# Kernel tuning notes

Measured on AMD Instinct MI355X. Metric: run time of the kernel, lower is better.

The kernel has to match this reference:

```python
import jax, jax.numpy as jnp
import numpy as np

N_HEAD = 12

def setup_inputs() -> dict:
    key = jax.random.key(0)
    ks = jax.random.split(key, 6)
    B, T, C, P = 8, 1024, 768, 4
    s = 0.02
    return {
        "x": jax.random.normal(ks[0], (B, T, C), jnp.float32),
        "kv_cvec": jax.random.normal(ks[1], (B, P, 2 * C), jnp.float32),
        "w_attn": jax.random.normal(ks[2], (C, 3 * C), jnp.float32) * s,
        "b_attn": jax.random.normal(ks[3], (3 * C,), jnp.float32) * s,
        "w_proj": jax.random.normal(ks[4], (C, C), jnp.float32) * s,
        "b_proj": jax.random.normal(ks[5], (C,), jnp.float32) * s,
    }

def reference(x, kv_cvec, w_attn, b_attn, w_proj, b_proj):
    B, T, C = x.shape
    P = kv_cvec.shape[1]
    D = C // N_HEAD

    # fused QKV projection
    qkv = x @ w_attn + b_attn                       # [B, T, 3C]
    q, k, v = jnp.split(qkv, 3, axis=-1)

    def to_heads(t):  # [B, S, C] -> [B, H, S, D]
        return t.reshape(t.shape[0], t.shape[1], N_HEAD, D).transpose(0, 2, 1, 3)

    q, k, v = to_heads(q), to_heads(k), to_heads(v)

    # prepend prefix (cvec) keys/values -> kv length T+P
    k_cvec, v_cvec = jnp.split(kv_cvec, 2, axis=-1)  # [B, P, C] each
    k = jnp.concatenate([to_heads(k_cvec), k], axis=2)
    v = jnp.concatenate([to_heads(v_cvec), v], axis=2)

    scale = 1.0 / jnp.sqrt(jnp.asarray(D, dtype=x.dtype))
    scores = jnp.einsum('bhqd,bhkd->bhqk', q, k) * scale  # [B,H,T,T+P]

    # mask: prefix columns fully visible, rest causal
    qi = jnp.arange(T)[:, None]
    kj = jnp.arange(T + P)[None, :]
    mask = (kj < P) | ((kj - P) <= qi)                     # [T, T+P]
    scores = jnp.where(mask, scores, jnp.finfo(scores.dtype).min)

    attn = jax.nn.softmax(scores, axis=-1)
    y = jnp.einsum('bhqk,bhkd->bhqd', attn, v)             # [B,H,T,D]
    y = y.transpose(0, 2, 1, 3).reshape(B, T, C)
    return y @ w_proj + b_proj
```

## Files before the change

### kernel.cpp

```cpp
#include <hip/hip_runtime.h>

#define BB 8
#define TT 1024
#define CC 768
#define HH 12
#define DD 64
#define PP 4
#define SS 1028
#define SP 1056

typedef unsigned short u16;
typedef __bf16 bf16x8 __attribute__((ext_vector_type(8)));
typedef unsigned short u16x8 __attribute__((ext_vector_type(8)));
typedef unsigned short u16x4 __attribute__((ext_vector_type(4)));
typedef float f32x4 __attribute__((ext_vector_type(4)));

__device__ __forceinline__ u16 f2bf(float f) {
  unsigned u = __float_as_uint(f);
  u += 0x7FFFu + ((u >> 16) & 1u);
  return (u16)(u >> 16);
}

__device__ __forceinline__ bf16x8 ldfrag(const u16* p) {
  u16x8 v = *reinterpret_cast<const u16x8*>(p);
  return __builtin_bit_cast(bf16x8, v);
}

__device__ __forceinline__ void gload16(const void* g, void* l) {
  __builtin_amdgcn_global_load_lds(
      (const __attribute__((address_space(1))) char*)g,
      (__attribute__((address_space(3))) char*)l, 16, 0, 0);
}

__global__ __launch_bounds__(256) void k_cast_x(const float* __restrict__ x,
                                                u16* __restrict__ xb) {
  int i = (blockIdx.x * 256 + threadIdx.x) * 8;
  float4 a = *reinterpret_cast<const float4*>(x + i);
  float4 b = *reinterpret_cast<const float4*>(x + i + 4);
  u16x8 o;
  o[0] = f2bf(a.x); o[1] = f2bf(a.y); o[2] = f2bf(a.z); o[3] = f2bf(a.w);
  o[4] = f2bf(b.x); o[5] = f2bf(b.y); o[6] = f2bf(b.z); o[7] = f2bf(b.w);
  *reinterpret_cast<u16x8*>(xb + i) = o;
}

__global__ __launch_bounds__(256) void k_transw(const float* __restrict__ w,
                                                u16* __restrict__ wt,
                                                int R, int Cc) {
  __shared__ u16 t[32][33];
  int tx = threadIdx.x & 31, ty = threadIdx.x >> 5;
  int r0 = blockIdx.y * 32, c0 = blockIdx.x * 32;
#pragma unroll
  for (int j = 0; j < 4; ++j) {
    int r = r0 + ty * 4 + j;
    t[ty * 4 + j][tx] = f2bf(w[(size_t)r * Cc + c0 + tx]);
  }
  __syncthreads();
#pragma unroll
  for (int j = 0; j < 4; ++j) {
    int c = c0 + ty * 4 + j;
    wt[(size_t)c * R + r0 + tx] = t[tx][ty * 4 + j];
  }
}

__global__ __launch_bounds__(256) void k_prefix(const float* __restrict__ kv,
                                                u16* __restrict__ Ko,
                                                u16* __restrict__ Vo) {
  int idx = blockIdx.x * 256 + threadIdx.x;
  int which = idx >= (BB * PP * CC);
  int r = idx - which * (BB * PP * CC);
  int b = r / (PP * CC);
  int rem = r - b * (PP * CC);
  int p = rem / CC, c = rem - (rem / CC) * CC;
  int h = c >> 6, d = c & 63;
  float v = kv[(size_t)(b * PP + p) * (2 * CC) + which * CC + c];
  u16* dst = which ? Vo : Ko;
  dst[((size_t)(b * HH + h) * SP + p) * DD + d] = f2bf(v);
}

__global__ __launch_bounds__(256) void k_transv(const u16* __restrict__ V,
                                                u16* __restrict__ VT) {
  __shared__ u16 t[32][33];
  int tx = threadIdx.x & 31, ty = threadIdx.x >> 5;
  int bh = blockIdx.x >> 1, dt = blockIdx.x & 1;
  int s0 = blockIdx.y * 32;
  const u16* src = V + (size_t)bh * SP * DD;
  u16* dst = VT + (size_t)bh * DD * SP;
#pragma unroll
  for (int j = 0; j < 4; ++j)
    t[ty * 4 + j][tx] = src[(size_t)(s0 + ty * 4 + j) * DD + dt * 32 + tx];
  __syncthreads();
#pragma unroll
  for (int j = 0; j < 4; ++j)
    dst[(size_t)(dt * 32 + ty * 4 + j) * SP + s0 + tx] = t[tx][ty * 4 + j];
}

template <int MODE>
__global__ __launch_bounds__(256) void k_gemm(const u16* __restrict__ A,
                                              const u16* __restrict__ Bt,
                                              const float* __restrict__ bias,
                                              u16* __restrict__ Qo,
                                              u16* __restrict__ Ko,
                                              u16* __restrict__ Vo,
                                              float* __restrict__ Fo) {
  __shared__ u16 S[16384];
  u16* const As = S;
  u16* const Bs = S + 8192;

  const int tid = threadIdx.x;
  const int lane = tid & 63, wave = tid >> 6;
  const int wr = wave >> 1, wc = wave & 1;
  const int fr = lane & 15, fq = lane >> 4;
  const int mbase = blockIdx.x * 128, nbase = blockIdx.y * 128;
  const int n0 = nbase + wc * 64;

  f32x4 acc[4][4] = {};

  const int srow = wave * 32 + (lane >> 3);
  const int scol = (lane & 7) * 8;
  const u16* Ag = A + (size_t)(mbase + srow) * 768 + scol;
  const u16* Bg = Bt + (size_t)(nbase + srow) * 768 + scol;
  u16* const Asw = As + (wave * 32) * 64;
  u16* const Bsw = Bs + (wave * 32) * 64;

  for (int kt = 0; kt < 12; ++kt) {
#pragma unroll
    for (int j = 0; j < 4; ++j) {
      gload16(Ag + (size_t)j * 8 * 768 + kt * 64, Asw + j * 8 * 64);
      gload16(Bg + (size_t)j * 8 * 768 + kt * 64, Bsw + j * 8 * 64);
    }
    __syncthreads();
#pragma unroll
    for (int ks = 0; ks < 2; ++ks) {
      bf16x8 av[4], bv[4];
#pragma unroll
      for (int mi = 0; mi < 4; ++mi)
        av[mi] = ldfrag(As + (wr * 64 + mi * 16 + fr) * 64 + ks * 32 + fq * 8);
#pragma unroll
      for (int ni = 0; ni < 4; ++ni)
        bv[ni] = ldfrag(Bs + (wc * 64 + ni * 16 + fr) * 64 + ks * 32 + fq * 8);
#pragma unroll
      for (int mi = 0; mi < 4; ++mi)
#pragma unroll
        for (int ni = 0; ni < 4; ++ni)
          acc[mi][ni] = __builtin_amdgcn_mfma_f32_16x16x32_bf16(
              av[mi], bv[ni], acc[mi][ni], 0, 0, 0);
    }
    __syncthreads();
  }

  float bvl[4];
#pragma unroll
  for (int ni = 0; ni < 4; ++ni) bvl[ni] = bias[n0 + ni * 16 + fr];

  if (MODE == 0) {
    char* const W = (char*)S + wave * 4608;
    const int sec = n0 / 768;
    const int hd = (n0 - sec * 768) >> 6;
    u16* const base = (sec == 0) ? Qo : (sec == 1 ? Ko : Vo);
    const int sstr = (sec == 0) ? TT : SP;
    const int soff = (sec == 0) ? 0 : PP;
#pragma unroll
    for (int p = 0; p < 2; ++p) {
#pragma unroll
      for (int mi2 = 0; mi2 < 2; ++mi2)
#pragma unroll
        for (int ni = 0; ni < 4; ++ni)
#pragma unroll
          for (int i = 0; i < 4; ++i) {
            int lr = mi2 * 16 + fq * 4 + i;
            *(u16*)(W + lr * 144 + (ni * 16 + fr) * 2) =
                f2bf(acc[p * 2 + mi2][ni][i] + bvl[ni]);
          }
#pragma unroll
      for (int it = 0; it < 4; ++it) {
        int lr = it * 8 + (lane >> 3);
        u16x8 v = *(u16x8*)(W + lr * 144 + (lane & 7) * 16);
        int m = mbase + wr * 64 + p * 32 + lr;
        int b = m >> 10, t = m & 1023;
        *(u16x8*)(base + ((size_t)(b * HH + hd) * sstr + soff + t) * DD +
                  (lane & 7) * 8) = v;
      }
    }
  } else {
    char* const W = (char*)S + wave * 4352;
#pragma unroll
    for (int p = 0; p < 4; ++p) {
#pragma unroll
      for (int ni = 0; ni < 4; ++ni)
#pragma unroll
        for (int i = 0; i < 4; ++i) {
          int lr = fq * 4 + i;
          *(float*)(W + lr * 272 + (ni * 16 + fr) * 4) = acc[p][ni][i] + bvl[ni];
        }
#pragma unroll
      for (int it = 0; it < 4; ++it) {
        int lr = it * 4 + (lane >> 4);
        f32x4 v = *(f32x4*)(W + lr * 272 + (lane & 15) * 16);
        int m = mbase + wr * 64 + p * 16 + lr;
        *(f32x4*)(Fo + (size_t)m * 768 + n0 + (lane & 15) * 4) = v;
      }
    }
  }
}

__global__ __launch_bounds__(256) void k_attn(const u16* __restrict__ Q,
                                              const u16* __restrict__ K,
                                              const u16* __restrict__ VT,
                                              u16* __restrict__ Y) {
  __shared__ u16 Ks[2][4096];
  __shared__ u16 Vs[2][4096];
  __shared__ u16 Ps[4][2048];

  const int tid = threadIdx.x;
  const int lane = tid & 63, wave = tid >> 6;
  const int fr = lane & 15, fq = lane >> 4;
  const int tier = blockIdx.x / 96;
  const int bh = blockIdx.x - tier * 96;
  const int tile = 7 - tier;
  const int b = bh / HH, h = bh - b * HH;
  const int qw = tile * 128 + wave * 32;
  const int nblk = 2 * tile + 3;

  const u16* Qb = Q + ((size_t)bh * TT + qw) * DD;
  const u16* Kb = K + (size_t)bh * SP * DD;
  const u16* Vb = VT + (size_t)bh * DD * SP;

  bf16x8 qB[2][2];
#pragma unroll
  for (int qf = 0; qf < 2; ++qf)
#pragma unroll
    for (int ks = 0; ks < 2; ++ks)
      qB[qf][ks] = ldfrag(Qb + (size_t)(qf * 16 + fr) * DD + ks * 32 + fq * 8);

  f32x4 oacc[2][4] = {};
  float mrun[2] = {-1e30f, -1e30f};
  float lrun[2] = {0.f, 0.f};
  const float CSC = 0.125f * 1.44269504f;

  auto stage = [&](int buf, int kv0) {
#pragma unroll
    for (int i = 0; i < 2; ++i) {
      int g = i * 4 + wave;
      int t = g >> 1, ks = g & 1;
      int row = kv0 + t * 16 + fr;
      if (row > SP - 1) row = SP - 1;
      gload16(Kb + (size_t)row * DD + ks * 32 + fq * 8, &Ks[buf][g * 512]);
    }
#pragma unroll
    for (int i = 0; i < 2; ++i) {
      int g = i * 4 + wave;
      int dc = g >> 1, kc = g & 1;
      int col = kv0 + kc * 32 + fq * 8;
      if (col > SP - 8) col = SP - 8;
      gload16(Vb + (size_t)(dc * 16 + fr) * SP + col, &Vs[buf][g * 512]);
    }
  };

  stage(0, 0);
  __syncthreads();

  for (int blk = 0; blk < nblk; ++blk) {
    const int cur = blk & 1;
    const int kv0 = blk * 64;
    if (blk + 1 < nblk) stage(cur ^ 1, kv0 + 64);

    const bool active = (kv0 <= qw + 31 + PP);
    if (active) {
      f32x4 s[2][4] = {};
#pragma unroll
      for (int t = 0; t < 4; ++t) {
        bf16x8 k0 = ldfrag(&Ks[cur][(t * 2 + 0) * 512 + lane * 8]);
        bf16x8 k1 = ldfrag(&Ks[cur][(t * 2 + 1) * 512 + lane * 8]);
#pragma unroll
        for (int qf = 0; qf < 2; ++qf) {
          s[qf][t] = __builtin_amdgcn_mfma_f32_16x16x32_bf16(k0, qB[qf][0], s[qf][t], 0, 0, 0);
          s[qf][t] = __builtin_amdgcn_mfma_f32_16x16x32_bf16(k1, qB[qf][1], s[qf][t], 0, 0, 0);
        }
      }

      const bool needmask = (kv0 + 63 > qw + PP);
#pragma unroll
      for (int qf = 0; qf < 2; ++qf) {
        const int qrow = qw + qf * 16 + fr;
        if (needmask) {
#pragma unroll
          for (int t = 0; t < 4; ++t)
#pragma unroll
            for (int i = 0; i < 4; ++i) {
              int col = kv0 + t * 16 + fq * 4 + i;
              if (col > qrow + PP) s[qf][t][i] = -1e30f;
            }
        }
        float m16 = s[qf][0][0];
#pragma unroll
        for (int t = 0; t < 4; ++t)
#pragma unroll
          for (int i = 0; i < 4; ++i) m16 = fmaxf(m16, s[qf][t][i]);
        m16 = fmaxf(m16, __shfl_xor(m16, 16));
        m16 = fmaxf(m16, __shfl_xor(m16, 32));
        const float mnew = fmaxf(mrun[qf], m16);
        const float alr = __builtin_exp2f((mrun[qf] - mnew) * CSC);
        mrun[qf] = mnew;
        const float mc = mnew * CSC;

        float rs = 0.f;
#pragma unroll
        for (int t = 0; t < 4; ++t) {
          u16x4 w4;
#pragma unroll
          for (int i = 0; i < 4; ++i) {
            float p = __builtin_exp2f(fmaf(s[qf][t][i], CSC, -mc));
            rs += p;
            w4[i] = f2bf(p);
          }
          int off = (qf * 2 + (t >> 1)) * 512 + ((t & 1) * 2 + (fq >> 1)) * 128 +
                    fr * 8 + (fq & 1) * 4;
          *reinterpret_cast<u16x4*>(&Ps[wave][off]) = w4;
        }
        rs += __shfl_xor(rs, 16);
        rs += __shfl_xor(rs, 32);
        lrun[qf] = lrun[qf] * alr + rs;

        float a0 = __shfl(alr, fq * 4 + 0);
        float a1 = __shfl(alr, fq * 4 + 1);
        float a2 = __shfl(alr, fq * 4 + 2);
        float a3 = __shfl(alr, fq * 4 + 3);
#pragma unroll
        for (int dc = 0; dc < 4; ++dc) {
          oacc[qf][dc][0] *= a0;
          oacc[qf][dc][1] *= a1;
          oacc[qf][dc][2] *= a2;
          oacc[qf][dc][3] *= a3;
        }
      }

      asm volatile("s_waitcnt lgkmcnt(0)" ::: "memory");
      bf16x8 pa[2][2];
#pragma unroll
      for (int qf = 0; qf < 2; ++qf)
#pragma unroll
        for (int kc = 0; kc < 2; ++kc)
          pa[qf][kc] = ldfrag(&Ps[wave][(qf * 2 + kc) * 512 + lane * 8]);
#pragma unroll
      for (int kc = 0; kc < 2; ++kc)
#pragma unroll
        for (int dc = 0; dc < 4; ++dc) {
          bf16x8 vf = ldfrag(&Vs[cur][(dc * 2 + kc) * 512 + lane * 8]);
#pragma unroll
          for (int qf = 0; qf < 2; ++qf)
            oacc[qf][dc] = __builtin_amdgcn_mfma_f32_16x16x32_bf16(
                pa[qf][kc], vf, oacc[qf][dc], 0, 0, 0);
        }
    }
    __syncthreads();
  }

#pragma unroll
  for (int qf = 0; qf < 2; ++qf) {
    float l0 = 1.f / __shfl(lrun[qf], fq * 4 + 0);
    float l1 = 1.f / __shfl(lrun[qf], fq * 4 + 1);
    float l2 = 1.f / __shfl(lrun[qf], fq * 4 + 2);
    float l3 = 1.f / __shfl(lrun[qf], fq * 4 + 3);
#pragma unroll
    for (int dc = 0; dc < 4; ++dc) {
      int q0 = qw + qf * 16 + fq * 4;
      u16* yp = Y + ((size_t)b * TT + q0) * CC + h * DD + dc * 16 + fr;
      yp[0 * CC] = f2bf(oacc[qf][dc][0] * l0);
      yp[1 * CC] = f2bf(oacc[qf][dc][1] * l1);
      yp[2 * CC] = f2bf(oacc[qf][dc][2] * l2);
      yp[3 * CC] = f2bf(oacc[qf][dc][3] * l3);
    }
  }
}

extern "C" void kernel_launch(void* const* d_in, const int* in_sizes, int n_in,
                              void* d_out, int out_size, void* d_ws, size_t ws_size,
                              hipStream_t stream) {
  const float* x      = (const float*)d_in[0];
  const float* kv     = (const float*)d_in[1];
  const float* w_attn = (const float*)d_in[2];
  const float* b_attn = (const float*)d_in[3];
  const float* w_proj = (const float*)d_in[4];
  const float* b_proj = (const float*)d_in[5];
  float* out = (float*)d_out;

  char* ws = (char*)d_ws;
  u16* xb  = (u16*)(ws + 0);
  u16* wat = (u16*)(ws + 12582912);
  u16* wpt = (u16*)(ws + 16121856);
  u16* Qb  = (u16*)(ws + 17301504);
  u16* Kb  = (u16*)(ws + 29884416);
  u16* Vb  = (u16*)(ws + 42860544);
  u16* VTb = (u16*)(ws + 55836672);
  u16* Yb  = (u16*)(ws + 68812800);

  k_cast_x<<<3072, 256, 0, stream>>>(x, xb);
  k_transw<<<dim3(72, 24), 256, 0, stream>>>(w_attn, wat, 768, 2304);
  k_transw<<<dim3(24, 24), 256, 0, stream>>>(w_proj, wpt, 768, 768);
  k_gemm<0><<<dim3(64, 18), 256, 0, stream>>>(xb, wat, b_attn, Qb, Kb, Vb, nullptr);
  k_prefix<<<192, 256, 0, stream>>>(kv, Kb, Vb);
  k_transv<<<dim3(192, 33), 256, 0, stream>>>(Vb, VTb);
  k_attn<<<768, 256, 0, stream>>>(Qb, Kb, VTb, Yb);
  k_gemm<1><<<dim3(64, 6), 256, 0, stream>>>(Yb, wpt, b_proj, nullptr, nullptr, nullptr, out);
}
```

Baseline: 216.8 us.

## Load K/V fragments directly from global memory and defer softmax rescaling in attention

The attention kernel no longer stages K and V tiles through double-buffered shared memory with block-wide barriers. Each wave now loads its MFMA fragments straight from global memory (relying on L2/L1 caching) and uses its own per-wave block count, so waves with shorter causal ranges stop early. It also skips the running-max rescale unless the new block max exceeds the old one by a threshold, and uses the hardware bf16 conversion. The risk is global-load latency that is no longer hidden by explicit prefetch, plus redundant global traffic across the four waves.

```diff
diff --git a/kernel.cpp b/kernel.cpp
--- a/kernel.cpp
+++ b/kernel.cpp
@@ -19,6 +19,11 @@
   unsigned u = __float_as_uint(f);
   u += 0x7FFFu + ((u >> 16) & 1u);
   return (u16)(u >> 16);
+}
+
+__device__ __forceinline__ u16 f2bf_fast(float f) {
+  __bf16 h = (__bf16)f;
+  return __builtin_bit_cast(u16, h);
 }
 
 __device__ __forceinline__ bf16x8 ldfrag(const u16* p) {
@@ -207,8 +212,6 @@
                                               const u16* __restrict__ K,
                                               const u16* __restrict__ VT,
                                               u16* __restrict__ Y) {
-  __shared__ u16 Ks[2][4096];
-  __shared__ u16 Vs[2][4096];
   __shared__ u16 Ps[4][2048];
 
   const int tid = threadIdx.x;
@@ -219,7 +222,7 @@
   const int tile = 7 - tier;
   const int b = bh / HH, h = bh - b * HH;
   const int qw = tile * 128 + wave * 32;
-  const int nblk = 2 * tile + 3;
+  const int nblk = (qw + 98) >> 6;
 
   const u16* Qb = Q + ((size_t)bh * TT + qw) * DD;
   const u16* Kb = K + (size_t)bh * SP * DD;
@@ -236,91 +239,51 @@
   float mrun[2] = {-1e30f, -1e30f};
   float lrun[2] = {0.f, 0.f};
   const float CSC = 0.125f * 1.44269504f;
-
-  auto stage = [&](int buf, int kv0) {
-#pragma unroll
-    for (int i = 0; i < 2; ++i) {
-      int g = i * 4 + wave;
-      int t = g >> 1, ks = g & 1;
-      int row = kv0 + t * 16 + fr;
-      if (row > SP - 1) row = SP - 1;
-      gload16(Kb + (size_t)row * DD + ks * 32 + fq * 8, &Ks[buf][g * 512]);
-    }
-#pragma unroll
-    for (int i = 0; i < 2; ++i) {
-      int g = i * 4 + wave;
-      int dc = g >> 1, kc = g & 1;
-      int col = kv0 + kc * 32 + fq * 8;
-      if (col > SP - 8) col = SP - 8;
-      gload16(Vb + (size_t)(dc * 16 + fr) * SP + col, &Vs[buf][g * 512]);
-    }
-  };
-
-  stage(0, 0);
-  __syncthreads();
+  const float THRN = 8.0f / CSC;
+  u16* const plw = Ps[wave];
 
   for (int blk = 0; blk < nblk; ++blk) {
-    const int cur = blk & 1;
     const int kv0 = blk * 64;
-    if (blk + 1 < nblk) stage(cur ^ 1, kv0 + 64);
-
-    const bool active = (kv0 <= qw + 31 + PP);
-    if (active) {
-      f32x4 s[2][4] = {};
-#pragma unroll
-      for (int t = 0; t < 4; ++t) {
-        bf16x8 k0 = ldfrag(&Ks[cur][(t * 2 + 0) * 512 + lane * 8]);
-        bf16x8 k1 = ldfrag(&Ks[cur][(t * 2 + 1) * 512 + lane * 8]);
-#pragma unroll
-        for (int qf = 0; qf < 2; ++qf) {
-          s[qf][t] = __builtin_amdgcn_mfma_f32_16x16x32_bf16(k0, qB[qf][0], s[qf][t], 0, 0, 0);
-          s[qf][t] = __builtin_amdgcn_mfma_f32_16x16x32_bf16(k1, qB[qf][1], s[qf][t], 0, 0, 0);
-        }
-      }
-
-      const bool needmask = (kv0 + 63 > qw + PP);
+
+    f32x4 s[2][4] = {};
+#pragma unroll
+    for (int t = 0; t < 4; ++t) {
+      const u16* kr = Kb + (size_t)(kv0 + t * 16 + fr) * DD + fq * 8;
+      bf16x8 k0 = ldfrag(kr);
+      bf16x8 k1 = ldfrag(kr + 32);
 #pragma unroll
       for (int qf = 0; qf < 2; ++qf) {
-        const int qrow = qw + qf * 16 + fr;
-        if (needmask) {
-#pragma unroll
-          for (int t = 0; t < 4; ++t)
-#pragma unroll
-            for (int i = 0; i < 4; ++i) {
-              int col = kv0 + t * 16 + fq * 4 + i;
-              if (col > qrow + PP) s[qf][t][i] = -1e30f;
-            }
-        }
-        float m16 = s[qf][0][0];
+        s[qf][t] = __builtin_amdgcn_mfma_f32_16x16x32_bf16(k0, qB[qf][0], s[qf][t], 0, 0, 0);
+        s[qf][t] = __builtin_amdgcn_mfma_f32_16x16x32_bf16(k1, qB[qf][1], s[qf][t], 0, 0, 0);
+      }
+    }
+
+    const bool needmask = (kv0 + 63 > qw + PP);
+#pragma unroll
+    for (int qf = 0; qf < 2; ++qf) {
+      const int qrow = qw + qf * 16 + fr;
+      if (needmask) {
 #pragma unroll
         for (int t = 0; t < 4; ++t)
 #pragma unroll
-          for (int i = 0; i < 4; ++i) m16 = fmaxf(m16, s[qf][t][i]);
-        m16 = fmaxf(m16, __shfl_xor(m16, 16));
-        m16 = fmaxf(m16, __shfl_xor(m16, 32));
+          for (int i = 0; i < 4; ++i) {
+            int col = kv0 + t * 16 + fq * 4 + i;
+            if (col > qrow + PP) s[qf][t][i] = -1e30f;
+          }
+      }
+      float m16 = s[qf][0][0];
+#pragma unroll
+      for (int t = 0; t < 4; ++t)
+#pragma unroll
+        for (int i = 0; i < 4; ++i) m16 = fmaxf(m16, s[qf][t][i]);
+      m16 = fmaxf(m16, __shfl_xor(m16, 16));
+      m16 = fmaxf(m16, __shfl_xor(m16, 32));
+
+      if (!__all(m16 <= mrun[qf] + THRN)) {
         const float mnew = fmaxf(mrun[qf], m16);
         const float alr = __builtin_exp2f((mrun[qf] - mnew) * CSC);
         mrun[qf] = mnew;
-        const float mc = mnew * CSC;
-
-        float rs = 0.f;
-#pragma unroll
-        for (int t = 0; t < 4; ++t) {
-          u16x4 w4;
-#pragma unroll
-          for (int i = 0; i < 4; ++i) {
-            float p = __builtin_exp2f(fmaf(s[qf][t][i], CSC, -mc));
-            rs += p;
-            w4[i] = f2bf(p);
-          }
-          int off = (qf * 2 + (t >> 1)) * 512 + ((t & 1) * 2 + (fq >> 1)) * 128 +
-                    fr * 8 + (fq & 1) * 4;
-          *reinterpret_cast<u16x4*>(&Ps[wave][off]) = w4;
-        }
-        rs += __shfl_xor(rs, 16);
-        rs += __shfl_xor(rs, 32);
-        lrun[qf] = lrun[qf] * alr + rs;
-
+        lrun[qf] *= alr;
         float a0 = __shfl(alr, fq * 4 + 0);
         float a1 = __shfl(alr, fq * 4 + 1);
         float a2 = __shfl(alr, fq * 4 + 2);
@@ -333,26 +296,44 @@
           oacc[qf][dc][3] *= a3;
         }
       }
-
-      asm volatile("s_waitcnt lgkmcnt(0)" ::: "memory");
-      bf16x8 pa[2][2];
-#pragma unroll
-      for (int qf = 0; qf < 2; ++qf)
-#pragma unroll
-        for (int kc = 0; kc < 2; ++kc)
-          pa[qf][kc] = ldfrag(&Ps[wave][(qf * 2 + kc) * 512 + lane * 8]);
+      const float mc = mrun[qf] * CSC;
+
+      float rs = 0.f;
+#pragma unroll
+      for (int t = 0; t < 4; ++t) {
+        u16x4 w4;
+#pragma unroll
+        for (int i = 0; i < 4; ++i) {
+          float p = __builtin_exp2f(fmaf(s[qf][t][i], CSC, -mc));
+          rs += p;
+          w4[i] = f2bf_fast(p);
+        }
+        int off = (qf * 2 + (t >> 1)) * 512 + ((t & 1) * 2 + (fq >> 1)) * 128 +
+                  fr * 8 + (fq & 1) * 4;
+        *reinterpret_cast<u16x4*>(&plw[off]) = w4;
+      }
+      rs += __shfl_xor(rs, 16);
+      rs += __shfl_xor(rs, 32);
+      lrun[qf] += rs;
+    }
+
+    asm volatile("s_waitcnt lgkmcnt(0)" ::: "memory");
+    bf16x8 pa[2][2];
+#pragma unroll
+    for (int qf = 0; qf < 2; ++qf)
 #pragma unroll
       for (int kc = 0; kc < 2; ++kc)
-#pragma unroll
-        for (int dc = 0; dc < 4; ++dc) {
-          bf16x8 vf = ldfrag(&Vs[cur][(dc * 2 + kc) * 512 + lane * 8]);
-#pragma unroll
-          for (int qf = 0; qf < 2; ++qf)
-            oacc[qf][dc] = __builtin_amdgcn_mfma_f32_16x16x32_bf16(
-                pa[qf][kc], vf, oacc[qf][dc], 0, 0, 0);
-        }
-    }
-    __syncthreads();
+        pa[qf][kc] = ldfrag(&plw[(qf * 2 + kc) * 512 + lane * 8]);
+#pragma unroll
+    for (int kc = 0; kc < 2; ++kc)
+#pragma unroll
+      for (int dc = 0; dc < 4; ++dc) {
+        bf16x8 vf = ldfrag(Vb + (size_t)(dc * 16 + fr) * SP + kv0 + kc * 32 + fq * 8);
+#pragma unroll
+        for (int qf = 0; qf < 2; ++qf)
+          oacc[qf][dc] = __builtin_amdgcn_mfma_f32_16x16x32_bf16(
+              pa[qf][kc], vf, oacc[qf][dc], 0, 0, 0);
+      }
   }
 
 #pragma unroll
@@ -365,10 +346,10 @@
     for (int dc = 0; dc < 4; ++dc) {
       int q0 = qw + qf * 16 + fq * 4;
       u16* yp = Y + ((size_t)b * TT + q0) * CC + h * DD + dc * 16 + fr;
-      yp[0 * CC] = f2bf(oacc[qf][dc][0] * l0);
-      yp[1 * CC] = f2bf(oacc[qf][dc][1] * l1);
-      yp[2 * CC] = f2bf(oacc[qf][dc][2] * l2);
-      yp[3 * CC] = f2bf(oacc[qf][dc][3] * l3);
+      yp[0 * CC] = f2bf_fast(oacc[qf][dc][0] * l0);
+      yp[1 * CC] = f2bf_fast(oacc[qf][dc][1] * l1);
+      yp[2 * CC] = f2bf_fast(oacc[qf][dc][2] * l2);
+      yp[3 * CC] = f2bf_fast(oacc[qf][dc][3] * l3);
     }
   }
 }
```

New measurement: 225.0 us. 1.04x slower.
